# Kernel tuning notes

Measured on AMD Instinct MI355X. Metric: run time of the kernel, lower is better.

The kernel has to match this reference:

```python
import jax, jax.numpy as jnp
import numpy as np
import math

N, T, NS, NO, HID = 256, 1000, 10, 10, 64


def gru_seq(x, Wi, Wh, bi, bh):
    # x: [N,T,D] -> hidden states [N,T,HID] (single-layer GRU, h0 = 0)
    xproj = x @ Wi + bi  # [N,T,3H], precompute input projections
    def step(h, xp):
        hp = h @ Wh + bh
        xr, xz, xn = jnp.split(xp, 3, axis=-1)
        hr, hz, hn = jnp.split(hp, 3, axis=-1)
        r = jax.nn.sigmoid(xr + hr)
        z = jax.nn.sigmoid(xz + hz)
        n = jnp.tanh(xn + r * hn)
        h_new = (1.0 - z) * n + z * h
        return h_new, h_new
    h0 = jnp.zeros((x.shape[0], Wh.shape[0]), x.dtype)
    _, hs = jax.lax.scan(step, h0, jnp.swapaxes(xproj, 0, 1))
    return jnp.swapaxes(hs, 0, 1)


def setup_inputs() -> dict:
    key = jax.random.key(0)
    ks = jax.random.split(key, 12)
    D = NO + NS  # GRU input = concat(y, x_hat)
    s = lambda fan: 1.0 / np.sqrt(fan)
    inp = {
        "Yi_batch": jax.random.normal(ks[0], (N, T, NO), jnp.float32),
        "X_hat_batch": jax.random.normal(ks[1], (N, T, NS), jnp.float32),
        # per-sample observation noise covariance: 0.5*I plus small random diagonal
        "Cw_batch": 0.5 * jnp.eye(NO, dtype=jnp.float32)[None] + jnp.eye(NO)[None] * 0.1 * jax.random.uniform(ks[2], (N, 1, 1), jnp.float32),
        "H": jax.random.normal(ks[3], (NO, NS), jnp.float32) * s(NS),
        "mu_w": jnp.zeros((NO, 1), jnp.float32),
        "Wi": jax.random.normal(ks[4], (D, 3 * HID), jnp.float32) * s(D),
        "Wh": jax.random.normal(ks[5], (HID, 3 * HID), jnp.float32) * s(HID),
        "bi": jnp.zeros((3 * HID,), jnp.float32),
        "bh": jnp.zeros((3 * HID,), jnp.float32),
        "W_mu": jax.random.normal(ks[6], (HID, NS), jnp.float32) * s(HID),
        "b_mu": jnp.zeros((NS,), jnp.float32),
        "W_var": jax.random.normal(ks[7], (HID, NS), jnp.float32) * s(HID),
        "b_var": jnp.zeros((NS,), jnp.float32),
    }
    return inp


def reference(Yi_batch, X_hat_batch, Cw_batch, H, mu_w, Wi, Wh, bi, bh, W_mu, b_mu, W_var, b_var):
    n_obs = Yi_batch.shape[-1]
    Tlen = Yi_batch.shape[1]
    # RNN: mu and (positive) vars per time step
    hs = gru_seq(jnp.concatenate([Yi_batch, X_hat_batch], axis=-1), Wi, Wh, bi, bh)
    mu_prev = hs @ W_mu + b_mu                       # [N,T,NS]
    var_prev = jax.nn.softplus(hs @ W_var + b_var)   # [N,T,NS] diag of L_xt_yt_prev
    # marginal over y: mu_y = H mu_prev + mu_w ; L_y = H diag(var) H^T + Cw
    mu_y = jnp.einsum('ij,ntj->nti', H, mu_prev) + mu_w[:, 0]
    HLH = jnp.einsum('ij,ntj,kj->ntik', H, var_prev, H)   # [N,T,NO,NO]
    L_y = HLH + Cw_batch[:, None]                          # broadcast Cw over time
    e = Yi_batch - mu_y
    # Gaussian log-likelihood via Cholesky (L_y is SPD)
    chol = jnp.linalg.cholesky(L_y)
    logdet = 2.0 * jnp.sum(jnp.log(jnp.diagonal(chol, axis1=-2, axis2=-1)), axis=-1)  # [N,T]
    sol = jnp.linalg.solve(L_y, e[..., None])[..., 0]
    quad = jnp.sum(e * sol, axis=-1)                       # [N,T]
    logprob = (-0.5 * n_obs * Tlen * math.log(2.0 * math.pi)
               - 0.5 * jnp.sum(logdet, axis=1)
               - 0.5 * jnp.sum(quad, axis=1))              # [N]
    return jnp.mean(logprob / (Tlen * n_obs))
```

## Files before the change

### kernel.cpp

```cpp
#include <hip/hip_runtime.h>
#include <math.h>

#define BN 256
#define TT 1000
#define NO 10
#define NS 10
#define HID 64
#define DIN 20
#define G3 192
#define WV 4
#define KW 16
#define GS 8
#define NG 125

__device__ __forceinline__ float bcast(float v, int l) {
    return __int_as_float(__builtin_amdgcn_readlane(__float_as_int(v), l));
}
__device__ __forceinline__ float rcpf(float x) { return __builtin_amdgcn_rcpf(x); }

__device__ __forceinline__ void sync_lds() {
    asm volatile("s_waitcnt lgkmcnt(0)\n\ts_barrier" ::: "memory");
}

__global__
__attribute__((amdgpu_flat_work_group_size(256, 256), amdgpu_waves_per_eu(1, 1)))
void gru_phase1(const float* __restrict__ Yi, const float* __restrict__ Xh,
                const float* __restrict__ Wi, const float* __restrict__ Wh,
                const float* __restrict__ bi, const float* __restrict__ bh,
                const float* __restrict__ Wmu, const float* __restrict__ Wvar,
                float* __restrict__ mv_out) {
    const int tid = threadIdx.x;
    const int lane = tid & 63;
    const int w = tid >> 6;
    const int kb = w * KW;

    __shared__ float4 part[2][WV][HID];
    __shared__ float pamv[2][WV][HID];
    __shared__ float inbuf[2][GS * DIN];
    __shared__ float obuf[2][GS * DIN];

    const int n = blockIdx.x;
    const float* ybase = Yi + (size_t)n * TT * NO;
    const float* xbase = Xh + (size_t)n * TT * NS;
    float* obase = mv_out + (size_t)n * TT * DIN;

    float whr[KW], whz[KW], whn[KW], wmv[KW];
    float wir[5], wiz[5], win[5];
#pragma unroll
    for (int k = 0; k < KW; ++k) {
        const int kk = kb + k;
        whr[k] = Wh[kk * G3 + lane];
        whz[k] = Wh[kk * G3 + 64 + lane];
        whn[k] = Wh[kk * G3 + 128 + lane];
        float wm = (lane < NS) ? Wmu[kk * NS + lane] : 0.0f;
        float wv = (lane >= NS && lane < 2 * NS) ? Wvar[kk * NS + (lane - NS)] : 0.0f;
        wmv[k] = wm + wv;
    }
#pragma unroll
    for (int k = 0; k < 5; ++k) {
        const int d = 5 * w + k;
        wir[k] = Wi[d * G3 + lane];
        wiz[k] = Wi[d * G3 + 64 + lane];
        win[k] = Wi[d * G3 + 128 + lane];
    }
    const float b_r  = bi[lane] + bh[lane];
    const float b_z  = bi[64 + lane] + bh[64 + lane];
    const float bx_n = bi[128 + lane];
    const float bh_n = bh[128 + lane];

    const int ibase = ((w >= 2) ? 80 : 0) + (w & 1) * 5;

    if (tid < 160)
        inbuf[0][tid] = (tid < 80) ? ybase[tid] : xbase[tid - 80];
    sync_lds();

    float h = 0.0f;

#pragma unroll 1
    for (int g = 0; g < NG; ++g) {
        float ld = 0.0f;
        const bool do_ld = (tid < 160) && (g + 1 < NG);
        if (do_ld)
            ld = (tid < 80) ? ybase[(size_t)(g + 1) * 80 + tid]
                            : xbase[(size_t)(g + 1) * 80 + (tid - 80)];
        const float* ib = inbuf[g & 1];

#pragma unroll
        for (int s = 0; s < GS; ++s) {
            const int ro = ibase + 10 * s;
            const float x0 = ib[ro], x1 = ib[ro + 1], x2 = ib[ro + 2];
            const float x3 = ib[ro + 3], x4 = ib[ro + 4];
            float pr = x0 * wir[0], pz = x0 * wiz[0], px = x0 * win[0];
            pr = fmaf(x1, wir[1], pr); pz = fmaf(x1, wiz[1], pz); px = fmaf(x1, win[1], px);
            pr = fmaf(x2, wir[2], pr); pz = fmaf(x2, wiz[2], pz); px = fmaf(x2, win[2], px);
            pr = fmaf(x3, wir[3], pr); pz = fmaf(x3, wiz[3], pz); px = fmaf(x3, win[3], px);
            pr = fmaf(x4, wir[4], pr); pz = fmaf(x4, wiz[4], pz); px = fmaf(x4, win[4], px);
            float pn = 0.0f, pm = 0.0f;
#pragma unroll
            for (int k = 0; k < KW; ++k) {
                float sv = bcast(h, kb + k);
                pr = fmaf(sv, whr[k], pr);
                pz = fmaf(sv, whz[k], pz);
                pn = fmaf(sv, whn[k], pn);
                pm = fmaf(sv, wmv[k], pm);
            }
            const int bufp = s & 1;
            part[bufp][w][lane] = make_float4(pr, pz, px, pn);
            pamv[bufp][w][lane] = pm;
            if (s == GS - 1 && do_ld) inbuf[(g + 1) & 1][tid] = ld;
            sync_lds();

            const float4 q0 = part[bufp][0][lane];
            const float4 q1 = part[bufp][1][lane];
            const float4 q2 = part[bufp][2][lane];
            const float4 q3 = part[bufp][3][lane];
            const float ar = b_r  + ((q0.x + q1.x) + (q2.x + q3.x));
            const float az = b_z  + ((q0.y + q1.y) + (q2.y + q3.y));
            const float ax = bx_n + ((q0.z + q1.z) + (q2.z + q3.z));
            const float ah = bh_n + ((q0.w + q1.w) + (q2.w + q3.w));
            if (w == 3) {
                float amv = (pamv[bufp][0][lane] + pamv[bufp][1][lane])
                          + (pamv[bufp][2][lane] + pamv[bufp][3][lane]);
                if (lane < DIN && !(g == 0 && s == 0)) {
                    const int tm1 = 8 * g + s - 1;
                    obuf[(tm1 >> 3) & 1][(tm1 & 7) * DIN + lane] = amv;
                }
            }
            if (s == 1 && g >= 1 && tid < 160)
                obase[(size_t)(g - 1) * 160 + tid] = obuf[(g - 1) & 1][tid];

            float r = rcpf(1.0f + __expf(-ar));
            float z = rcpf(1.0f + __expf(-az));
            float pre = fmaf(r, ah, ax);
            float e2 = __expf(2.0f * pre);
            float nn = 1.0f - 2.0f * rcpf(e2 + 1.0f);
            h = fmaf(z, h - nn, nn);
        }
    }

    {
        float pm = 0.0f;
#pragma unroll
        for (int k = 0; k < KW; ++k) pm = fmaf(bcast(h, kb + k), wmv[k], pm);
        pamv[0][w][lane] = pm;
        sync_lds();
        if (w == 3 && lane < DIN) {
            float amv = (pamv[0][0][lane] + pamv[0][1][lane])
                      + (pamv[0][2][lane] + pamv[0][3][lane]);
            obuf[0][7 * DIN + lane] = amv;
        }
        sync_lds();
        if (tid < 160)
            obase[(size_t)(NG - 1) * 160 + tid] = obuf[0][tid];
    }
}

__global__ void init_out(float* out) {
    out[0] = -0.918938533204672742f;
}

__global__ __launch_bounds__(256)
void lik_phase2(const float* __restrict__ Yi, const float* __restrict__ Cw,
                const float* __restrict__ Hm, const float* __restrict__ mu_w,
                const float* __restrict__ b_mu, const float* __restrict__ b_var,
                const float* __restrict__ mv_in, float* __restrict__ out) {
    __shared__ float sH[NO * NS];
    __shared__ float smw[NO], sbm[NS], sbv[NS];
    __shared__ float ssum[4];
    const int tid = threadIdx.x;
    if (tid < NO * NS) sH[tid] = Hm[tid];
    if (tid < NO) smw[tid] = mu_w[tid];
    if (tid < NS) { sbm[tid] = b_mu[tid]; sbv[tid] = b_var[tid]; }
    __syncthreads();

    const int gid = blockIdx.x * 256 + tid;
    float contrib = 0.0f;
    if (gid < BN * TT) {
        const int n = gid / TT;
        const float* mv = mv_in + (size_t)gid * DIN;
        float mu[NS], va[NS];
#pragma unroll
        for (int i = 0; i < NS; ++i) {
            mu[i] = mv[i] + sbm[i];
            float x = mv[NS + i] + sbv[i];
            va[i] = (x > 0.0f) ? (x + log1pf(__expf(-x))) : log1pf(__expf(x));
        }
        const float* y = Yi + (size_t)gid * NO;
        float e[NO];
#pragma unroll
        for (int i = 0; i < NO; ++i) {
            float m = smw[i];
#pragma unroll
            for (int j = 0; j < NS; ++j) m = fmaf(sH[i * NS + j], mu[j], m);
            e[i] = y[i] - m;
        }
        float M[NO][NO];
        const float* cw = Cw + (size_t)n * NO * NO;
#pragma unroll
        for (int i = 0; i < NO; ++i)
#pragma unroll
            for (int j = 0; j <= i; ++j) M[i][j] = cw[i * NO + j];
#pragma unroll
        for (int l = 0; l < NS; ++l) {
            float vl = va[l];
            float hv[NO];
#pragma unroll
            for (int i = 0; i < NO; ++i) hv[i] = sH[i * NS + l];
#pragma unroll
            for (int i = 0; i < NO; ++i) {
                float hvi = hv[i] * vl;
#pragma unroll
                for (int j = 0; j <= i; ++j) M[i][j] = fmaf(hvi, hv[j], M[i][j]);
            }
        }
        float logdet = 0.0f;
        float drs[NO];
#pragma unroll
        for (int j = 0; j < NO; ++j) {
            float d = M[j][j];
#pragma unroll
            for (int k = 0; k < j; ++k) d = fmaf(-M[j][k], M[j][k], d);
            logdet += __logf(d);
            float rs = __frsqrt_rn(d);
            drs[j] = rs;
            M[j][j] = d * rs;
#pragma unroll
            for (int i = j + 1; i < NO; ++i) {
                float v = M[i][j];
#pragma unroll
                for (int k = 0; k < j; ++k) v = fmaf(-M[i][k], M[j][k], v);
                M[i][j] = v * rs;
            }
        }
        float wv[NO];
        float quad = 0.0f;
#pragma unroll
        for (int i = 0; i < NO; ++i) {
            float v = e[i];
#pragma unroll
            for (int k = 0; k < i; ++k) v = fmaf(-M[i][k], wv[k], v);
            wv[i] = v * drs[i] * rcpf(M[i][i] * drs[i]);
            quad = fmaf(wv[i], wv[i], quad);
        }
        const float SCALE = 0.5f / ((float)BN * (float)TT * (float)NO);
        contrib = -(logdet + quad) * SCALE;
    }

#pragma unroll
    for (int off = 32; off > 0; off >>= 1) contrib += __shfl_down(contrib, off);
    if ((tid & 63) == 0) ssum[tid >> 6] = contrib;
    __syncthreads();
    if (tid == 0) {
        float s = ssum[0] + ssum[1] + ssum[2] + ssum[3];
        atomicAdd(out, s);
    }
}

extern "C" void kernel_launch(void* const* d_in, const int* in_sizes, int n_in,
                              void* d_out, int out_size, void* d_ws, size_t ws_size,
                              hipStream_t stream) {
    const float* Yi    = (const float*)d_in[0];
    const float* Xh    = (const float*)d_in[1];
    const float* Cw    = (const float*)d_in[2];
    const float* Hm    = (const float*)d_in[3];
    const float* mu_w  = (const float*)d_in[4];
    const float* Wi    = (const float*)d_in[5];
    const float* Wh    = (const float*)d_in[6];
    const float* bi    = (const float*)d_in[7];
    const float* bh    = (const float*)d_in[8];
    const float* W_mu  = (const float*)d_in[9];
    const float* b_mu  = (const float*)d_in[10];
    const float* W_var = (const float*)d_in[11];
    const float* b_var = (const float*)d_in[12];
    float* out = (float*)d_out;
    float* mv  = (float*)d_ws;

    init_out<<<1, 1, 0, stream>>>(out);
    gru_phase1<<<dim3(BN), dim3(256), 0, stream>>>(Yi, Xh, Wi, Wh, bi, bh,
                                                   W_mu, W_var, mv);
    lik_phase2<<<dim3((BN * TT + 255) / 256), dim3(256), 0, stream>>>(
        Yi, Cw, Hm, mu_w, b_mu, b_var, mv, out);
}
```

Measured before the change: 590.6 us.

## Move output projections out of the GRU recurrence into the likelihood kernel via fp16 hidden states

The serial GRU kernel no longer computes the mu/var output projections or stages inputs through LDS. It broadcasts inputs held in registers via readlane and writes each hidden state as fp16 to workspace. The likelihood kernel now does the 64x20 projection per timestep from LDS weights. This shortens the latency-bound recurrent step at the cost of more global traffic (64 halves instead of 20 floats per step) and fp16 rounding of the hidden state. The Cholesky path also drops a redundant reciprocal and uses one log of the diagonal product, and the init kernel is replaced by a memset plus a constant folded into block 0.

```diff
diff --git a/kernel.cpp b/kernel.cpp
--- a/kernel.cpp
+++ b/kernel.cpp
@@ -1,4 +1,5 @@
 #include <hip/hip_runtime.h>
+#include <hip/hip_fp16.h>
 #include <math.h>
 
 #define BN 256
@@ -12,6 +13,7 @@
 #define KW 16
 #define GS 8
 #define NG 125
+#define C_HALF_LOG2PI -0.918938533204672742f
 
 __device__ __forceinline__ float bcast(float v, int l) {
     return __int_as_float(__builtin_amdgcn_readlane(__float_as_int(v), l));
@@ -22,28 +24,263 @@
     asm volatile("s_waitcnt lgkmcnt(0)\n\ts_barrier" ::: "memory");
 }
 
+
 __global__
 __attribute__((amdgpu_flat_work_group_size(256, 256), amdgpu_waves_per_eu(1, 1)))
-void gru_phase1(const float* __restrict__ Yi, const float* __restrict__ Xh,
-                const float* __restrict__ Wi, const float* __restrict__ Wh,
-                const float* __restrict__ bi, const float* __restrict__ bh,
-                const float* __restrict__ Wmu, const float* __restrict__ Wvar,
-                float* __restrict__ mv_out) {
+void gru_h(const float* __restrict__ Yi, const float* __restrict__ Xh,
+           const float* __restrict__ Wi, const float* __restrict__ Wh,
+           const float* __restrict__ bi, const float* __restrict__ bh,
+           __half* __restrict__ hout) {
     const int tid = threadIdx.x;
     const int lane = tid & 63;
     const int w = tid >> 6;
     const int kb = w * KW;
 
     __shared__ float4 part[2][WV][HID];
+
+    const int n = blockIdx.x;
+    const float* ybase = Yi + (size_t)n * TT * NO;
+    const float* xbase = Xh + (size_t)n * TT * NS;
+    __half* hbase = hout + (size_t)n * TT * HID;
+
+    float whr[KW], whz[KW], whn[KW];
+#pragma unroll
+    for (int k = 0; k < KW; ++k) {
+        const int kk = kb + k;
+        whr[k] = Wh[kk * G3 + lane];
+        whz[k] = Wh[kk * G3 + 64 + lane];
+        whn[k] = Wh[kk * G3 + 128 + lane];
+    }
+    float wir[5], wiz[5], win[5];
+#pragma unroll
+    for (int k = 0; k < 5; ++k) {
+        const int d = 5 * w + k;
+        wir[k] = Wi[d * G3 + lane];
+        wiz[k] = Wi[d * G3 + 64 + lane];
+        win[k] = Wi[d * G3 + 128 + lane];
+    }
+    const float b_r  = bi[lane] + bh[lane];
+    const float b_z  = bi[64 + lane] + bh[64 + lane];
+    const float bx_n = bi[128 + lane];
+    const float bh_n = bh[128 + lane];
+
+    const float* src = (w < 2) ? ybase : xbase;
+    const int off5 = (w & 1) * 5;
+    const int ls = lane / 5;
+    const int ld = lane - 5 * ls;
+    const bool lact = (lane < 40);
+
+    float xcur = lact ? src[10 * ls + off5 + ld] : 0.0f;
+    float h = 0.0f;
+
+#pragma unroll 1
+    for (int g = 0; g < NG; ++g) {
+        float xnext = 0.0f;
+        if (lact && (g + 1) < NG)
+            xnext = src[(size_t)(g + 1) * 80 + 10 * ls + off5 + ld];
+
+#pragma unroll
+        for (int s = 0; s < GS; ++s) {
+            const int t = 8 * g + s;
+            const float x0 = bcast(xcur, 5 * s + 0);
+            const float x1 = bcast(xcur, 5 * s + 1);
+            const float x2 = bcast(xcur, 5 * s + 2);
+            const float x3 = bcast(xcur, 5 * s + 3);
+            const float x4 = bcast(xcur, 5 * s + 4);
+            float pr = x0 * wir[0], pz = x0 * wiz[0], px = x0 * win[0];
+            pr = fmaf(x1, wir[1], pr); pz = fmaf(x1, wiz[1], pz); px = fmaf(x1, win[1], px);
+            pr = fmaf(x2, wir[2], pr); pz = fmaf(x2, wiz[2], pz); px = fmaf(x2, win[2], px);
+            pr = fmaf(x3, wir[3], pr); pz = fmaf(x3, wiz[3], pz); px = fmaf(x3, win[3], px);
+            pr = fmaf(x4, wir[4], pr); pz = fmaf(x4, wiz[4], pz); px = fmaf(x4, win[4], px);
+            float pn = 0.0f;
+#pragma unroll
+            for (int k = 0; k < KW; ++k) {
+                float sv = bcast(h, kb + k);
+                pr = fmaf(sv, whr[k], pr);
+                pz = fmaf(sv, whz[k], pz);
+                pn = fmaf(sv, whn[k], pn);
+            }
+            const int bufp = s & 1;
+            part[bufp][w][lane] = make_float4(pr, pz, px, pn);
+            sync_lds();
+
+            const float4 q0 = part[bufp][0][lane];
+            const float4 q1 = part[bufp][1][lane];
+            const float4 q2 = part[bufp][2][lane];
+            const float4 q3 = part[bufp][3][lane];
+            const float ar = b_r  + ((q0.x + q1.x) + (q2.x + q3.x));
+            const float az = b_z  + ((q0.y + q1.y) + (q2.y + q3.y));
+            const float ax = bx_n + ((q0.z + q1.z) + (q2.z + q3.z));
+            const float ah = bh_n + ((q0.w + q1.w) + (q2.w + q3.w));
+            float r = rcpf(1.0f + __expf(-ar));
+            float z = rcpf(1.0f + __expf(-az));
+            float pre = fmaf(r, ah, ax);
+            float e2 = __expf(2.0f * pre);
+            float nn = 1.0f - 2.0f * rcpf(e2 + 1.0f);
+            h = fmaf(z, h - nn, nn);
+            if (w == 0)
+                hbase[(size_t)t * HID + lane] = __float2half(h);
+        }
+        xcur = xnext;
+    }
+}
+
+__global__ __launch_bounds__(256)
+void lik_h(const float* __restrict__ Yi, const float* __restrict__ Cw,
+           const float* __restrict__ Hm, const float* __restrict__ mu_w,
+           const float* __restrict__ Wmu, const float* __restrict__ b_mu,
+           const float* __restrict__ Wvar, const float* __restrict__ b_var,
+           const __half* __restrict__ hbuf, float* __restrict__ out) {
+    __shared__ float sWm[HID][12];
+    __shared__ float sWv[HID][12];
+    __shared__ float sH[NO * NS];
+    __shared__ float smw[NO], sbm[NS], sbv[NS];
+    __shared__ float ssum[4];
+    const int tid = threadIdx.x;
+    for (int i = tid; i < HID * NS; i += 256) {
+        sWm[i / NS][i % NS] = Wmu[i];
+        sWv[i / NS][i % NS] = Wvar[i];
+    }
+    if (tid < NO * NS) sH[tid] = Hm[tid];
+    if (tid < NO) smw[tid] = mu_w[tid];
+    if (tid < NS) { sbm[tid] = b_mu[tid]; sbv[tid] = b_var[tid]; }
+    __syncthreads();
+
+    const int gid = blockIdx.x * 256 + tid;
+    float contrib = 0.0f;
+    if (gid < BN * TT) {
+        const int n = gid / TT;
+        float mu[NS], va[NS];
+#pragma unroll
+        for (int i = 0; i < NS; ++i) { mu[i] = sbm[i]; va[i] = sbv[i]; }
+        const uint4* hp = (const uint4*)(hbuf + (size_t)gid * HID);
+#pragma unroll
+        for (int c = 0; c < 8; ++c) {
+            const uint4 u = hp[c];
+            float hk[8];
+            float2 f;
+            f = __half22float2(*(const __half2*)&u.x); hk[0] = f.x; hk[1] = f.y;
+            f = __half22float2(*(const __half2*)&u.y); hk[2] = f.x; hk[3] = f.y;
+            f = __half22float2(*(const __half2*)&u.z); hk[4] = f.x; hk[5] = f.y;
+            f = __half22float2(*(const __half2*)&u.w); hk[6] = f.x; hk[7] = f.y;
+#pragma unroll
+            for (int j = 0; j < 8; ++j) {
+                const int k = 8 * c + j;
+                const float x = hk[j];
+                const float4 m0 = *(const float4*)&sWm[k][0];
+                const float4 m1 = *(const float4*)&sWm[k][4];
+                const float2 m2 = *(const float2*)&sWm[k][8];
+                const float4 v0 = *(const float4*)&sWv[k][0];
+                const float4 v1 = *(const float4*)&sWv[k][4];
+                const float2 v2 = *(const float2*)&sWv[k][8];
+                mu[0] = fmaf(x, m0.x, mu[0]); mu[1] = fmaf(x, m0.y, mu[1]);
+                mu[2] = fmaf(x, m0.z, mu[2]); mu[3] = fmaf(x, m0.w, mu[3]);
+                mu[4] = fmaf(x, m1.x, mu[4]); mu[5] = fmaf(x, m1.y, mu[5]);
+                mu[6] = fmaf(x, m1.z, mu[6]); mu[7] = fmaf(x, m1.w, mu[7]);
+                mu[8] = fmaf(x, m2.x, mu[8]); mu[9] = fmaf(x, m2.y, mu[9]);
+                va[0] = fmaf(x, v0.x, va[0]); va[1] = fmaf(x, v0.y, va[1]);
+                va[2] = fmaf(x, v0.z, va[2]); va[3] = fmaf(x, v0.w, va[3]);
+                va[4] = fmaf(x, v1.x, va[4]); va[5] = fmaf(x, v1.y, va[5]);
+                va[6] = fmaf(x, v1.z, va[6]); va[7] = fmaf(x, v1.w, va[7]);
+                va[8] = fmaf(x, v2.x, va[8]); va[9] = fmaf(x, v2.y, va[9]);
+            }
+        }
+#pragma unroll
+        for (int i = 0; i < NS; ++i) {
+            float x = va[i];
+            va[i] = (x > 0.0f) ? (x + log1pf(__expf(-x))) : log1pf(__expf(x));
+        }
+        const float* y = Yi + (size_t)gid * NO;
+        float e[NO];
+#pragma unroll
+        for (int i = 0; i < NO; ++i) {
+            float m = smw[i];
+#pragma unroll
+            for (int j = 0; j < NS; ++j) m = fmaf(sH[i * NS + j], mu[j], m);
+            e[i] = y[i] - m;
+        }
+        float M[NO][NO];
+        const float* cw = Cw + (size_t)n * NO * NO;
+#pragma unroll
+        for (int i = 0; i < NO; ++i)
+#pragma unroll
+            for (int j = 0; j <= i; ++j) M[i][j] = cw[i * NO + j];
+#pragma unroll
+        for (int l = 0; l < NS; ++l) {
+            float vl = va[l];
+            float hv[NO];
+#pragma unroll
+            for (int i = 0; i < NO; ++i) hv[i] = sH[i * NS + l];
+#pragma unroll
+            for (int i = 0; i < NO; ++i) {
+                float hvi = hv[i] * vl;
+#pragma unroll
+                for (int j = 0; j <= i; ++j) M[i][j] = fmaf(hvi, hv[j], M[i][j]);
+            }
+        }
+        float dprod = 1.0f;
+        float drs[NO];
+#pragma unroll
+        for (int j = 0; j < NO; ++j) {
+            float d = M[j][j];
+#pragma unroll
+            for (int k = 0; k < j; ++k) d = fmaf(-M[j][k], M[j][k], d);
+            dprod *= d;
+            float rs = __frsqrt_rn(d);
+            drs[j] = rs;
+#pragma unroll
+            for (int i = j + 1; i < NO; ++i) {
+                float v = M[i][j];
+#pragma unroll
+                for (int k = 0; k < j; ++k) v = fmaf(-M[i][k], M[j][k], v);
+                M[i][j] = v * rs;
+            }
+        }
+        const float logdet = __logf(dprod);
+        float wv[NO];
+        float quad = 0.0f;
+#pragma unroll
+        for (int i = 0; i < NO; ++i) {
+            float v = e[i];
+#pragma unroll
+            for (int k = 0; k < i; ++k) v = fmaf(-M[i][k], wv[k], v);
+            wv[i] = v * drs[i];
+            quad = fmaf(wv[i], wv[i], quad);
+        }
+        const float SCALE = 0.5f / ((float)BN * (float)TT * (float)NO);
+        contrib = -(logdet + quad) * SCALE;
+    }
+
+#pragma unroll
+    for (int off = 32; off > 0; off >>= 1) contrib += __shfl_down(contrib, off);
+    if ((tid & 63) == 0) ssum[tid >> 6] = contrib;
+    __syncthreads();
+    if (tid == 0) {
+        float s = ssum[0] + ssum[1] + ssum[2] + ssum[3];
+        if (blockIdx.x == 0) s += C_HALF_LOG2PI;
+        atomicAdd(out, s);
+    }
+}
+
+__global__
+__attribute__((amdgpu_flat_work_group_size(256, 256), amdgpu_waves_per_eu(1, 1)))
+void gru_fb(const float* __restrict__ Yi, const float* __restrict__ Xh,
+            const float* __restrict__ Wi, const float* __restrict__ Wh,
+            const float* __restrict__ bi, const float* __restrict__ bh,
+            const float* __restrict__ Wmu, const float* __restrict__ Wvar,
+            float* __restrict__ mv_out) {
+    const int tid = threadIdx.x;
+    const int lane = tid & 63;
+    const int w = tid >> 6;
+    const int kb = w * KW;
+    __shared__ float4 part[2][WV][HID];
     __shared__ float pamv[2][WV][HID];
     __shared__ float inbuf[2][GS * DIN];
     __shared__ float obuf[2][GS * DIN];
-
     const int n = blockIdx.x;
     const float* ybase = Yi + (size_t)n * TT * NO;
     const float* xbase = Xh + (size_t)n * TT * NS;
     float* obase = mv_out + (size_t)n * TT * DIN;
-
     float whr[KW], whz[KW], whn[KW], wmv[KW];
     float wir[5], wiz[5], win[5];
 #pragma unroll
@@ -53,8 +290,8 @@
         whz[k] = Wh[kk * G3 + 64 + lane];
         whn[k] = Wh[kk * G3 + 128 + lane];
         float wm = (lane < NS) ? Wmu[kk * NS + lane] : 0.0f;
-        float wv = (lane >= NS && lane < 2 * NS) ? Wvar[kk * NS + (lane - NS)] : 0.0f;
-        wmv[k] = wm + wv;
+        float wvv = (lane >= NS && lane < 2 * NS) ? Wvar[kk * NS + (lane - NS)] : 0.0f;
+        wmv[k] = wm + wvv;
     }
 #pragma unroll
     for (int k = 0; k < 5; ++k) {
@@ -67,15 +304,11 @@
     const float b_z  = bi[64 + lane] + bh[64 + lane];
     const float bx_n = bi[128 + lane];
     const float bh_n = bh[128 + lane];
-
     const int ibase = ((w >= 2) ? 80 : 0) + (w & 1) * 5;
-
     if (tid < 160)
         inbuf[0][tid] = (tid < 80) ? ybase[tid] : xbase[tid - 80];
     sync_lds();
-
     float h = 0.0f;
-
 #pragma unroll 1
     for (int g = 0; g < NG; ++g) {
         float ld = 0.0f;
@@ -84,7 +317,6 @@
             ld = (tid < 80) ? ybase[(size_t)(g + 1) * 80 + tid]
                             : xbase[(size_t)(g + 1) * 80 + (tid - 80)];
         const float* ib = inbuf[g & 1];
-
 #pragma unroll
         for (int s = 0; s < GS; ++s) {
             const int ro = ibase + 10 * s;
@@ -109,7 +341,6 @@
             pamv[bufp][w][lane] = pm;
             if (s == GS - 1 && do_ld) inbuf[(g + 1) & 1][tid] = ld;
             sync_lds();
-
             const float4 q0 = part[bufp][0][lane];
             const float4 q1 = part[bufp][1][lane];
             const float4 q2 = part[bufp][2][lane];
@@ -128,7 +359,6 @@
             }
             if (s == 1 && g >= 1 && tid < 160)
                 obase[(size_t)(g - 1) * 160 + tid] = obuf[(g - 1) & 1][tid];
-
             float r = rcpf(1.0f + __expf(-ar));
             float z = rcpf(1.0f + __expf(-az));
             float pre = fmaf(r, ah, ax);
@@ -137,7 +367,6 @@
             h = fmaf(z, h - nn, nn);
         }
     }
-
     {
         float pm = 0.0f;
 #pragma unroll
@@ -155,15 +384,11 @@
     }
 }
 
-__global__ void init_out(float* out) {
-    out[0] = -0.918938533204672742f;
-}
-
 __global__ __launch_bounds__(256)
-void lik_phase2(const float* __restrict__ Yi, const float* __restrict__ Cw,
-                const float* __restrict__ Hm, const float* __restrict__ mu_w,
-                const float* __restrict__ b_mu, const float* __restrict__ b_var,
-                const float* __restrict__ mv_in, float* __restrict__ out) {
+void lik_fb(const float* __restrict__ Yi, const float* __restrict__ Cw,
+            const float* __restrict__ Hm, const float* __restrict__ mu_w,
+            const float* __restrict__ b_mu, const float* __restrict__ b_var,
+            const float* __restrict__ mv_in, float* __restrict__ out) {
     __shared__ float sH[NO * NS];
     __shared__ float smw[NO], sbm[NS], sbv[NS];
     __shared__ float ssum[4];
@@ -172,7 +397,6 @@
     if (tid < NO) smw[tid] = mu_w[tid];
     if (tid < NS) { sbm[tid] = b_mu[tid]; sbv[tid] = b_var[tid]; }
     __syncthreads();
-
     const int gid = blockIdx.x * 256 + tid;
     float contrib = 0.0f;
     if (gid < BN * TT) {
@@ -213,17 +437,16 @@
                 for (int j = 0; j <= i; ++j) M[i][j] = fmaf(hvi, hv[j], M[i][j]);
             }
         }
-        float logdet = 0.0f;
+        float dprod = 1.0f;
         float drs[NO];
 #pragma unroll
         for (int j = 0; j < NO; ++j) {
             float d = M[j][j];
 #pragma unroll
             for (int k = 0; k < j; ++k) d = fmaf(-M[j][k], M[j][k], d);
-            logdet += __logf(d);
+            dprod *= d;
             float rs = __frsqrt_rn(d);
             drs[j] = rs;
-            M[j][j] = d * rs;
 #pragma unroll
             for (int i = j + 1; i < NO; ++i) {
                 float v = M[i][j];
@@ -232,6 +455,7 @@
                 M[i][j] = v * rs;
             }
         }
+        const float logdet = __logf(dprod);
         float wv[NO];
         float quad = 0.0f;
 #pragma unroll
@@ -239,19 +463,19 @@
             float v = e[i];
 #pragma unroll
             for (int k = 0; k < i; ++k) v = fmaf(-M[i][k], wv[k], v);
-            wv[i] = v * drs[i] * rcpf(M[i][i] * drs[i]);
+            wv[i] = v * drs[i];
             quad = fmaf(wv[i], wv[i], quad);
         }
         const float SCALE = 0.5f / ((float)BN * (float)TT * (float)NO);
         contrib = -(logdet + quad) * SCALE;
     }
-
 #pragma unroll
     for (int off = 32; off > 0; off >>= 1) contrib += __shfl_down(contrib, off);
     if ((tid & 63) == 0) ssum[tid >> 6] = contrib;
     __syncthreads();
     if (tid == 0) {
         float s = ssum[0] + ssum[1] + ssum[2] + ssum[3];
+        if (blockIdx.x == 0) s += C_HALF_LOG2PI;
         atomicAdd(out, s);
     }
 }
@@ -273,11 +497,20 @@
     const float* W_var = (const float*)d_in[11];
     const float* b_var = (const float*)d_in[12];
     float* out = (float*)d_out;
-    float* mv  = (float*)d_ws;
-
-    init_out<<<1, 1, 0, stream>>>(out);
-    gru_phase1<<<dim3(BN), dim3(256), 0, stream>>>(Yi, Xh, Wi, Wh, bi, bh,
+
+    hipMemsetAsync(d_out, 0, sizeof(float), stream);
+
+    const size_t need_h = (size_t)BN * TT * HID * sizeof(__half);
+    if (ws_size >= need_h) {
+        __half* hbuf = (__half*)d_ws;
+        gru_h<<<dim3(BN), dim3(256), 0, stream>>>(Yi, Xh, Wi, Wh, bi, bh, hbuf);
+        lik_h<<<dim3((BN * TT + 255) / 256), dim3(256), 0, stream>>>(
+            Yi, Cw, Hm, mu_w, W_mu, b_mu, W_var, b_var, hbuf, out);
+    } else {
+        float* mv = (float*)d_ws;
+        gru_fb<<<dim3(BN), dim3(256), 0, stream>>>(Yi, Xh, Wi, Wh, bi, bh,
                                                    W_mu, W_var, mv);
-    lik_phase2<<<dim3((BN * TT + 255) / 256), dim3(256), 0, stream>>>(
-        Yi, Cw, Hm, mu_w, b_mu, b_var, mv, out);
-}
+        lik_fb<<<dim3((BN * TT + 255) / 256), dim3(256), 0, stream>>>(
+            Yi, Cw, Hm, mu_w, b_mu, b_var, mv, out);
+    }
+}
```

New measurement: 1.147 ms. 1.94x slower.
